# Optimization experiments

Hardware: AMD Instinct MI355X
Metric: run time of the kernel (lower is better)

Reference implementation:

```python
import jax, jax.numpy as jnp
import numpy as np

N = 50000   # nodes
E = 800000  # edges
B = 512     # graphs
EPS = 1e-5  # BatchNorm eps


def _p(k, shape, scale=0.05):
    return jax.random.normal(k, shape, dtype=jnp.float32) * scale


def setup_inputs() -> dict:
    key = jax.random.key(0)
    ks = jax.random.split(key, 24)
    inp = {
        "x": jax.random.normal(ks[0], (N, 4), dtype=jnp.float32),
        "edge_index": jax.random.randint(ks[1], (2, E), 0, N, dtype=jnp.int64),
        "edge_weight": jax.random.uniform(ks[2], (E,), dtype=jnp.float32),
        "batch": jnp.sort(jax.random.randint(ks[3], (N,), 0, B, dtype=jnp.int64)),
        # block1: GCNConv(4,64) + BN + shortcut Linear(4,64)
        "W1": _p(ks[4], (4, 64)), "b1": jnp.zeros((64,), jnp.float32),
        "g1": jnp.ones((64,), jnp.float32), "be1": jnp.zeros((64,), jnp.float32),
        "sW1": _p(ks[5], (4, 64)), "sb1": jnp.zeros((64,), jnp.float32),
        # block2: GCNConv(64,64) + BN, identity shortcut
        "W2": _p(ks[6], (64, 64)), "b2": jnp.zeros((64,), jnp.float32),
        "g2": jnp.ones((64,), jnp.float32), "be2": jnp.zeros((64,), jnp.float32),
        # block3: GCNConv(64,128) + BN + shortcut Linear(64,128)
        "W3": _p(ks[7], (64, 128)), "b3": jnp.zeros((128,), jnp.float32),
        "g3": jnp.ones((128,), jnp.float32), "be3": jnp.zeros((128,), jnp.float32),
        "sW3": _p(ks[8], (64, 128)), "sb3": jnp.zeros((128,), jnp.float32),
        # head: Linear(256,128) + BN + ReLU + Linear(128,1)
        "fW1": _p(ks[9], (256, 128)), "fb1": jnp.zeros((128,), jnp.float32),
        "fg": jnp.ones((128,), jnp.float32), "fbe": jnp.zeros((128,), jnp.float32),
        "fW2": _p(ks[10], (128, 1)), "fb2": jnp.zeros((1,), jnp.float32),
    }
    return inp


def _bn(x, g, b):
    # training-mode BatchNorm1d over node dim (biased variance)
    m = x.mean(0)
    v = x.var(0)
    return (x - m) * jax.lax.rsqrt(v + EPS) * g + b


def _gcn(x, W, b, src, dst, w, n):
    # PyG GCNConv: add self-loops (weight 1), symmetric normalization
    h = x @ W  # [n, out]
    loop = jnp.arange(n)
    s = jnp.concatenate([src, loop])
    d = jnp.concatenate([dst, loop])
    ww = jnp.concatenate([w, jnp.ones((n,), x.dtype)])
    deg = jax.ops.segment_sum(ww, d, num_segments=n)
    dis = jnp.where(deg > 0, jax.lax.rsqrt(jnp.maximum(deg, EPS)), 0.0)
    norm = dis[s] * ww * dis[d]  # [E+n]
    return jax.ops.segment_sum(h[s] * norm[:, None], d, num_segments=n) + b


def _block(x, W, b, g, be, sW, sb, src, dst, w, n):
    out = jax.nn.relu(_bn(_gcn(x, W, b, src, dst, w, n), g, be))
    sc = x if sW is None else x @ sW + sb
    return out + sc


def reference(x, edge_index, edge_weight, batch,
              W1, b1, g1, be1, sW1, sb1,
              W2, b2, g2, be2,
              W3, b3, g3, be3, sW3, sb3,
              fW1, fb1, fg, fbe, fW2, fb2):
    n = x.shape[0]
    src, dst = edge_index[0], edge_index[1]
    h = _block(x, W1, b1, g1, be1, sW1, sb1, src, dst, edge_weight, n)
    h = _block(h, W2, b2, g2, be2, None, None, src, dst, edge_weight, n)
    h = _block(h, W3, b3, g3, be3, sW3, sb3, src, dst, edge_weight, n)
    # global mean / max pooling per graph
    cnt = jax.ops.segment_sum(jnp.ones((n,), h.dtype), batch, num_segments=B)
    p1 = jax.ops.segment_sum(h, batch, num_segments=B) / jnp.maximum(cnt, 1.0)[:, None]
    p2 = jax.ops.segment_max(h, batch, num_segments=B)
    z = jnp.concatenate([p1, p2], axis=1)  # [B, 256]
    z = jax.nn.relu(_bn(z @ fW1 + fb1, fg, fbe))  # Dropout eval = identity
    return z @ fW2 + fb2  # [B, 1]
```

## Files before the change

### kernel.cpp

```cpp
#include <hip/hip_runtime.h>
#include <hip/hip_fp16.h>

#define BNEPS 1e-5f


__global__ void k_fill(float* p, int n, float v){
  int i = blockIdx.x*blockDim.x + threadIdx.x;
  if(i < n) p[i] = v;
}


__global__ void k_count(int* cnt, int* rank, const int* __restrict__ dst, int E){
  int e = blockIdx.x*blockDim.x + threadIdx.x;
  if(e < E) rank[e] = atomicAdd(&cnt[dst[e]], 1);
}

__global__ void k_scan1(const int* __restrict__ cnt, int* rowptr, int* bsum, int n){
  __shared__ int sh[256];
  int tid = threadIdx.x;
  int i = blockIdx.x*256 + tid;
  int v = (i < n) ? cnt[i] : 0;
  sh[tid] = v;
  __syncthreads();
  for(int o = 1; o < 256; o <<= 1){
    int t = (tid >= o) ? sh[tid-o] : 0;
    __syncthreads();
    sh[tid] += t;
    __syncthreads();
  }
  if(i < n) rowptr[i] = sh[tid] - v;
  if(tid == 255) bsum[blockIdx.x] = sh[255];
}

__global__ void k_scan2(int* bsum, int m){
  __shared__ int sh[256];
  int tid = threadIdx.x;
  int v = (tid < m) ? bsum[tid] : 0;
  sh[tid] = v;
  __syncthreads();
  for(int o = 1; o < 256; o <<= 1){
    int t = (tid >= o) ? sh[tid-o] : 0;
    __syncthreads();
    sh[tid] += t;
    __syncthreads();
  }
  if(tid < m) bsum[tid] = sh[tid] - v;
}

__global__ void k_scan3(int* rowptr, const int* bsum, int n, int E){
  int i = blockIdx.x*blockDim.x + threadIdx.x;
  if(i < n) rowptr[i] += bsum[i >> 8];
  if(i == 0) rowptr[n] = E;
}

__global__ void k_scatter2(const int* __restrict__ src, const int* __restrict__ dst,
                           const float* __restrict__ w, const int* __restrict__ rowptr,
                           const int* __restrict__ rank, int2* __restrict__ erec, int E){
  int e = blockIdx.x*blockDim.x + threadIdx.x;
  if(e >= E) return;
  int d = dst[e];
  erec[rowptr[d] + rank[e]] = make_int2(src[e], __float_as_int(w[e]));
}

__global__ void k_degdis(const int2* __restrict__ erec, const int* __restrict__ rowptr,
                         float* __restrict__ dis, int n){
  int i = blockIdx.x*blockDim.x + threadIdx.x;
  if(i >= n) return;
  float s = 1.0f;
  int e0 = rowptr[i], e1 = rowptr[i+1];
  for(int j = e0; j < e1; j++) s += __int_as_float(erec[j].y);
  dis[i] = rsqrtf(s);
}

__global__ void k_mknorm(int2* __restrict__ erec, const int* __restrict__ rowptr,
                         const float* __restrict__ dis, int n){
  int i = blockIdx.x*blockDim.x + threadIdx.x;
  if(i >= n) return;
  float di = dis[i];
  int e0 = rowptr[i], e1 = rowptr[i+1];
  for(int j = e0; j < e1; j++){
    int2 r = erec[j];
    erec[j].y = __float_as_int(dis[r.x] * __int_as_float(r.y) * di);
  }
}


__global__ __launch_bounds__(256)
void k_gcn1_fused(const float* __restrict__ X, const float* __restrict__ dis,
                  const int* __restrict__ rowptr, const int2* __restrict__ erec,
                  const float* __restrict__ W, const float* __restrict__ bias,
                  float* __restrict__ H, float* __restrict__ st1s, int n){
  const int tid = threadIdx.x;
  const int lane = tid & 63;
  const int wid = tid >> 6;
  const int eg = lane >> 2;
  const int ch = lane & 3;
  const float w0 = W[lane], w1 = W[64+lane], w2 = W[128+lane], w3 = W[192+lane];
  const float bc = bias[lane];
  float s = 0.f, s2 = 0.f;
  for(int i = blockIdx.x*4 + wid; i < n; i += gridDim.x*4){
    int e0 = rowptr[i], e1 = rowptr[i+1];
    float acc = 0.f;
    for(int j = e0 + eg; j < e1; j += 16){
      int2 r = erec[j];
      acc += X[(size_t)r.x*4 + ch] * __int_as_float(r.y);
    }
    if(eg == 0){
      float d = dis[i];
      acc += X[(size_t)i*4 + ch] * d * d;
    }
    acc += __shfl_xor(acc, 4);
    acc += __shfl_xor(acc, 8);
    acc += __shfl_xor(acc, 16);
    acc += __shfl_xor(acc, 32);
    float p0 = __shfl(acc, 0), p1 = __shfl(acc, 1);
    float p2 = __shfl(acc, 2), p3 = __shfl(acc, 3);
    float h = bc + p0*w0 + p1*w1 + p2*w2 + p3*w3;
    H[(size_t)i*64 + lane] = h;
    s += h; s2 += h*h;
  }
  __shared__ float rs[256], rs2[256];
  rs[tid] = s; rs2[tid] = s2;
  __syncthreads();
  if(tid < 64){
    float* stp = st1s + (blockIdx.x & 7)*128;
    atomicAdd(&stp[tid],    rs[tid]+rs[tid+64]+rs[tid+128]+rs[tid+192]);
    atomicAdd(&stp[64+tid], rs2[tid]+rs2[tid+64]+rs2[tid+128]+rs2[tid+192]);
  }
}


__global__ void k_gather64h(const __half* __restrict__ H, const float* __restrict__ dis,
                            const int* __restrict__ rowptr, const int2* __restrict__ erec,
                            float* __restrict__ P, int n){
  int i = blockIdx.x*4 + threadIdx.x / 64;
  int c = threadIdx.x & 63;
  if(i >= n) return;
  float di = dis[i];
  float acc = __half2float(H[(size_t)i*64 + c])*di*di;
  int e0 = rowptr[i], e1 = rowptr[i+1];
  int j = e0;
  for(; j + 8 <= e1; j += 8){
    int2 r0 = erec[j],   r1 = erec[j+1], r2 = erec[j+2], r3 = erec[j+3];
    int2 r4 = erec[j+4], r5 = erec[j+5], r6 = erec[j+6], r7 = erec[j+7];
    float h0 = __half2float(H[(size_t)r0.x*64 + c]);
    float h1 = __half2float(H[(size_t)r1.x*64 + c]);
    float h2 = __half2float(H[(size_t)r2.x*64 + c]);
    float h3 = __half2float(H[(size_t)r3.x*64 + c]);
    float h4 = __half2float(H[(size_t)r4.x*64 + c]);
    float h5 = __half2float(H[(size_t)r5.x*64 + c]);
    float h6 = __half2float(H[(size_t)r6.x*64 + c]);
    float h7 = __half2float(H[(size_t)r7.x*64 + c]);
    acc += h0*__int_as_float(r0.y) + h1*__int_as_float(r1.y)
         + h2*__int_as_float(r2.y) + h3*__int_as_float(r3.y)
         + h4*__int_as_float(r4.y) + h5*__int_as_float(r5.y)
         + h6*__int_as_float(r6.y) + h7*__int_as_float(r7.y);
  }
  for(; j < e1; j++){
    int2 r = erec[j];
    acc += __half2float(H[(size_t)r.x*64 + c]) * __int_as_float(r.y);
  }
  P[(size_t)i*64 + c] = acc;
}


template<int C>
__global__ __launch_bounds__(256)
void k_gemm_tile(const float* __restrict__ X, const float* __restrict__ W,
                 const float* __restrict__ bias, float* __restrict__ H,
                 float* __restrict__ stats, int n, int ntiles){
  const int RR = C/16;
  const int CG = C/4;
  __shared__ float Xs[64*65];
  __shared__ float Ws[64*C];
  __shared__ float sst[2*C];
  const int tid = threadIdx.x;
  const int cg = tid % CG, rg = tid / CG;
  const int c0 = cg*4;
  for(int t = tid; t < 16*C; t += 256)
    reinterpret_cast<float4*>(Ws)[t] = reinterpret_cast<const float4*>(W)[t];
  const float4 bc = *reinterpret_cast<const float4*>(bias + c0);
  float sacc[4] = {0,0,0,0}, qacc[4] = {0,0,0,0};
  const float4* X4 = reinterpret_cast<const float4*>(X);
  for(int tile = blockIdx.x; tile < ntiles; tile += gridDim.x){
    const int r0 = tile*64;
    __syncthreads();
    #pragma unroll
    for(int q = 0; q < 4; q++){
      int idx = tid + q*256;
      int row = idx >> 4, k4 = idx & 15;
      float4 v = (r0+row < n) ? X4[(size_t)(r0+row)*16 + k4] : make_float4(0.f,0.f,0.f,0.f);
      Xs[(4*k4+0)*65 + row] = v.x;
      Xs[(4*k4+1)*65 + row] = v.y;
      Xs[(4*k4+2)*65 + row] = v.z;
      Xs[(4*k4+3)*65 + row] = v.w;
    }
    __syncthreads();
    float acc[RR][4];
    #pragma unroll
    for(int r = 0; r < RR; r++){ acc[r][0]=bc.x; acc[r][1]=bc.y; acc[r][2]=bc.z; acc[r][3]=bc.w; }
    #pragma unroll 8
    for(int k = 0; k < 64; k++){
      float4 wv = reinterpret_cast<const float4*>(Ws)[k*CG + cg];
      #pragma unroll
      for(int r = 0; r < RR; r++){
        float xv = Xs[k*65 + rg*RR + r];
        acc[r][0] = fmaf(xv, wv.x, acc[r][0]);
        acc[r][1] = fmaf(xv, wv.y, acc[r][1]);
        acc[r][2] = fmaf(xv, wv.z, acc[r][2]);
        acc[r][3] = fmaf(xv, wv.w, acc[r][3]);
      }
    }
    #pragma unroll
    for(int r = 0; r < RR; r++){
      int row = r0 + rg*RR + r;
      if(row < n){
        *reinterpret_cast<float4*>(H + (size_t)row*C + c0) =
            make_float4(acc[r][0], acc[r][1], acc[r][2], acc[r][3]);
        #pragma unroll
        for(int j = 0; j < 4; j++){ sacc[j] += acc[r][j]; qacc[j] += acc[r][j]*acc[r][j]; }
      }
    }
  }
  for(int t = tid; t < 2*C; t += 256) sst[t] = 0.f;
  __syncthreads();
  #pragma unroll
  for(int j = 0; j < 4; j++){
    atomicAdd(&sst[c0+j], sacc[j]);
    atomicAdd(&sst[C+c0+j], qacc[j]);
  }
  __syncthreads();
  for(int t = tid; t < 2*C; t += 256) atomicAdd(&stats[t], sst[t]);
}

__global__ __launch_bounds__(256)
void k_gemm_bnsc_tile_h(const __half* __restrict__ Xh, const float* __restrict__ sW,
                        const float* __restrict__ sb,
                        const float* __restrict__ agg, const float* __restrict__ stats,
                        const float* __restrict__ g, const float* __restrict__ be,
                        float* __restrict__ out, int n, int ntiles){
  const int C = 128, RR = 8, CG = 32;
  __shared__ float Xs[64*65];
  __shared__ float Ws[64*C];
  const int tid = threadIdx.x;
  const int cg = tid % CG, rg = tid / CG;
  const int c0 = cg*4;
  for(int t = tid; t < 16*C; t += 256)
    reinterpret_cast<float4*>(Ws)[t] = reinterpret_cast<const float4*>(sW)[t];
  const float4 bc = *reinterpret_cast<const float4*>(sb + c0);
  float scal[4], shft[4];
  {
    float invn = 1.0f / n;
    #pragma unroll
    for(int j = 0; j < 4; j++){
      float m = stats[c0+j]*invn;
      float v = stats[C+c0+j]*invn - m*m;
      float rs = rsqrtf(v + BNEPS) * g[c0+j];
      scal[j] = rs;
      shft[j] = be[c0+j] - m*rs;
    }
  }
  for(int tile = blockIdx.x; tile < ntiles; tile += gridDim.x){
    const int r0 = tile*64;
    __syncthreads();
    #pragma unroll
    for(int q = 0; q < 2; q++){
      int t = tid + q*256;
      int row = t >> 3, h8 = t & 7;
      float4 raw = make_float4(0.f,0.f,0.f,0.f);
      if(r0+row < n) raw = *reinterpret_cast<const float4*>(Xh + (size_t)(r0+row)*64 + h8*8);
      const __half2* hp = reinterpret_cast<const __half2*>(&raw);
      #pragma unroll
      for(int p = 0; p < 4; p++){
        float2 f = __half22float2(hp[p]);
        Xs[(h8*8 + 2*p    )*65 + row] = f.x;
        Xs[(h8*8 + 2*p + 1)*65 + row] = f.y;
      }
    }
    __syncthreads();
    float acc[RR][4];
    #pragma unroll
    for(int r = 0; r < RR; r++){ acc[r][0]=bc.x; acc[r][1]=bc.y; acc[r][2]=bc.z; acc[r][3]=bc.w; }
    #pragma unroll 8
    for(int k = 0; k < 64; k++){
      float4 wv = reinterpret_cast<const float4*>(Ws)[k*CG + cg];
      #pragma unroll
      for(int r = 0; r < RR; r++){
        float xv = Xs[k*65 + rg*RR + r];
        acc[r][0] = fmaf(xv, wv.x, acc[r][0]);
        acc[r][1] = fmaf(xv, wv.y, acc[r][1]);
        acc[r][2] = fmaf(xv, wv.z, acc[r][2]);
        acc[r][3] = fmaf(xv, wv.w, acc[r][3]);
      }
    }
    #pragma unroll
    for(int r = 0; r < RR; r++){
      int row = r0 + rg*RR + r;
      if(row < n){
        float4 a = *reinterpret_cast<const float4*>(agg + (size_t)row*C + c0);
        float4 o;
        o.x = fmaxf(a.x*scal[0] + shft[0], 0.f) + acc[r][0];
        o.y = fmaxf(a.y*scal[1] + shft[1], 0.f) + acc[r][1];
        o.z = fmaxf(a.z*scal[2] + shft[2], 0.f) + acc[r][2];
        o.w = fmaxf(a.w*scal[3] + shft[3], 0.f) + acc[r][3];
        *reinterpret_cast<float4*>(out + (size_t)row*C + c0) = o;
      }
    }
  }
}


__global__ void k_bn_add4_h(const float* __restrict__ agg, const float* __restrict__ stats,
                            const float* __restrict__ g, const float* __restrict__ be,
                            __half* __restrict__ buf, int n){
  int idx = blockIdx.x*blockDim.x + threadIdx.x;
  if(idx >= n*16) return;
  int c = (idx & 15)*4;
  float invn = 1.0f / n;
  float4 sm = *reinterpret_cast<const float4*>(stats + c);
  float4 sq = *reinterpret_cast<const float4*>(stats + 64 + c);
  float4 g4 = *reinterpret_cast<const float4*>(g + c);
  float4 b4 = *reinterpret_cast<const float4*>(be + c);
  float4 a  = reinterpret_cast<const float4*>(agg)[idx];
  __half2* bp = reinterpret_cast<__half2*>(buf) + idx*2;
  float2 ad01 = __half22float2(bp[0]);
  float2 ad23 = __half22float2(bp[1]);
  float o0,o1,o2,o3;
  { float m=sm.x*invn, v=sq.x*invn-m*m; o0 = fmaxf((a.x-m)*rsqrtf(v+BNEPS)*g4.x+b4.x,0.f)+ad01.x; }
  { float m=sm.y*invn, v=sq.y*invn-m*m; o1 = fmaxf((a.y-m)*rsqrtf(v+BNEPS)*g4.y+b4.y,0.f)+ad01.y; }
  { float m=sm.z*invn, v=sq.z*invn-m*m; o2 = fmaxf((a.z-m)*rsqrtf(v+BNEPS)*g4.z+b4.z,0.f)+ad23.x; }
  { float m=sm.w*invn, v=sq.w*invn-m*m; o3 = fmaxf((a.w-m)*rsqrtf(v+BNEPS)*g4.w+b4.w,0.f)+ad23.y; }
  bp[0] = __floats2half2_rn(o0,o1);
  bp[1] = __floats2half2_rn(o2,o3);
}

__global__ void k_bn_sc4_h(const float* __restrict__ agg, const float* __restrict__ st1s,
                           const float* __restrict__ g, const float* __restrict__ be,
                           const float* __restrict__ X, const float* __restrict__ sW,
                           const float* __restrict__ sb, __half* __restrict__ out, int n){
  int idx = blockIdx.x*blockDim.x + threadIdx.x;
  if(idx >= n*16) return;
  int i = idx >> 4;
  int c = (idx & 15)*4;
  float invn = 1.0f / n;
  float4 xr = *reinterpret_cast<const float4*>(X + (size_t)i*4);
  float4 s0 = *reinterpret_cast<const float4*>(sW + c);
  float4 s1 = *reinterpret_cast<const float4*>(sW + 64 + c);
  float4 s2 = *reinterpret_cast<const float4*>(sW + 128 + c);
  float4 s3 = *reinterpret_cast<const float4*>(sW + 192 + c);
  float4 sb4 = *reinterpret_cast<const float4*>(sb + c);
  float4 sm = make_float4(0.f,0.f,0.f,0.f), sq = make_float4(0.f,0.f,0.f,0.f);
  #pragma unroll
  for(int sh = 0; sh < 8; sh++){
    float4 a4 = *reinterpret_cast<const float4*>(st1s + sh*128 + c);
    float4 b4 = *reinterpret_cast<const float4*>(st1s + sh*128 + 64 + c);
    sm.x += a4.x; sm.y += a4.y; sm.z += a4.z; sm.w += a4.w;
    sq.x += b4.x; sq.y += b4.y; sq.z += b4.z; sq.w += b4.w;
  }
  float4 g4 = *reinterpret_cast<const float4*>(g + c);
  float4 b4 = *reinterpret_cast<const float4*>(be + c);
  float4 a  = reinterpret_cast<const float4*>(agg)[idx];
  float o0,o1,o2,o3;
  #define BN1(X_, O_) { float sc = xr.x*s0.X_ + xr.y*s1.X_ + xr.z*s2.X_ + xr.w*s3.X_ + sb4.X_; \
    float m = sm.X_*invn; float v = sq.X_*invn - m*m; \
    O_ = fmaxf((a.X_-m)*rsqrtf(v+BNEPS)*g4.X_ + b4.X_, 0.f) + sc; }
  BN1(x,o0) BN1(y,o1) BN1(z,o2) BN1(w,o3)
  #undef BN1
  __half2* op = reinterpret_cast<__half2*>(out) + idx*2;
  op[0] = __floats2half2_rn(o0,o1);
  op[1] = __floats2half2_rn(o2,o3);
}


__global__ void k_pool(const float* __restrict__ H, const int* __restrict__ batch,
                       float* __restrict__ z, int n){
  int b = blockIdx.x, c = threadIdx.x;
  int lo = 0, hi = n;
  while(lo < hi){ int mid = (lo+hi)>>1; if(batch[mid] <  b) lo = mid+1; else hi = mid; }
  int start = lo;
  hi = n;
  while(lo < hi){ int mid = (lo+hi)>>1; if(batch[mid] <  b+1) lo = mid+1; else hi = mid; }
  int end = lo;
  float s = 0.f, mx = -INFINITY;
  for(int i = start; i < end; i++){
    float v = H[(size_t)i*128 + c];
    s += v; mx = fmaxf(mx, v);
  }
  int cnt = end - start;
  z[b*256 + c]       = s / fmaxf((float)cnt, 1.f);
  z[b*256 + 128 + c] = mx;
}

__global__ void k_head1(const float* __restrict__ z, const float* __restrict__ fW1,
                        const float* __restrict__ fb1, float* __restrict__ zr,
                        float* __restrict__ stats, int B){
  int idx = blockIdx.x*blockDim.x + threadIdx.x;
  int tid = threadIdx.x;
  float acc = 0.f;
  if(idx < B*128){
    int b = idx >> 7, c = idx & 127;
    acc = fb1[c];
    #pragma unroll 4
    for(int k = 0; k < 256; k++) acc = fmaf(z[b*256+k], fW1[k*128+c], acc);
    zr[idx] = acc;
  }
  __shared__ float rs[256], rs2[256];
  rs[tid] = acc; rs2[tid] = acc*acc;
  __syncthreads();
  if(tid < 128){
    atomicAdd(&stats[tid],     rs[tid]+rs[tid+128]);
    atomicAdd(&stats[128+tid], rs2[tid]+rs2[tid+128]);
  }
}

__global__ void k_final(const float* __restrict__ zr, const float* __restrict__ stats,
                        const float* __restrict__ fg, const float* __restrict__ fbe,
                        const float* __restrict__ fW2, const float* __restrict__ fb2,
                        float* __restrict__ out, int B){
  __shared__ float red[128];
  int b = blockIdx.x, c = threadIdx.x;
  float invn = 1.0f / B;
  float m  = stats[c]*invn;
  float v  = stats[128+c]*invn - m*m;
  float rs = rsqrtf(v + BNEPS);
  float val = fmaxf((zr[b*128+c]-m)*rs*fg[c] + fbe[c], 0.f) * fW2[c];
  red[c] = val;
  __syncthreads();
  for(int s = 64; s > 0; s >>= 1){
    if(c < s) red[c] += red[c+s];
    __syncthreads();
  }
  if(c == 0) out[b] = red[0] + fb2[0];
}


extern "C" void kernel_launch(void* const* d_in, const int* in_sizes, int n_in,
                              void* d_out, int out_size, void* d_ws, size_t ws_size,
                              hipStream_t stream){
  const float* x   = (const float*)d_in[0];
  const int*   ei  = (const int*)  d_in[1];
  const float* ew  = (const float*)d_in[2];
  const int*   bat = (const int*)  d_in[3];
  const float* W1  = (const float*)d_in[4];  const float* b1  = (const float*)d_in[5];
  const float* g1  = (const float*)d_in[6];  const float* be1 = (const float*)d_in[7];
  const float* sW1 = (const float*)d_in[8];  const float* sb1 = (const float*)d_in[9];
  const float* W2  = (const float*)d_in[10]; const float* b2  = (const float*)d_in[11];
  const float* g2  = (const float*)d_in[12]; const float* be2 = (const float*)d_in[13];
  const float* W3  = (const float*)d_in[14]; const float* b3  = (const float*)d_in[15];
  const float* g3  = (const float*)d_in[16]; const float* be3 = (const float*)d_in[17];
  const float* sW3 = (const float*)d_in[18]; const float* sb3 = (const float*)d_in[19];
  const float* fW1 = (const float*)d_in[20]; const float* fb1 = (const float*)d_in[21];
  const float* fg  = (const float*)d_in[22]; const float* fbe = (const float*)d_in[23];
  const float* fW2 = (const float*)d_in[24]; const float* fb2 = (const float*)d_in[25];
  float* out = (float*)d_out;

  const int n = in_sizes[0] / 4;
  const int E = in_sizes[2];
  const int B = out_size;
  const int* src = ei;
  const int* dst = ei + E;

  auto GB = [](long long t){ return (int)((t + 255) / 256); };
  const int nscanb = (n + 255) / 256;
  const int ntiles = (n + 63) / 64;

  float* ws = (float*)d_ws;
  size_t off = 0;
  auto alloc = [&](size_t cnt)->float*{ float* p = ws + off; off += (cnt + 63) & ~size_t(63); return p; };

  const size_t npad = ((size_t)n + 63) & ~size_t(63);
  __half* bufA = (__half*)alloc((size_t)n * 32);
  float* hbuf  = alloc((size_t)n * 128);
  float* agg   = alloc((size_t)n * 128);
  float* z     = alloc((size_t)B * 256);
  float* zr    = alloc((size_t)B * 128);
  float* zreg  = alloc(npad + 1024 + 768);
  int*   cnt   = (int*)zreg;
  float* st1s = zreg + npad;
  float* st2  = st1s + 1024;
  float* st3  = st2 + 256;
  float* stH  = st3 + 256;
  float* dis    = alloc(n);
  int*   rowptr = (int*)alloc(n + 1);
  int*   bsum   = (int*)alloc(256);
  int*   rank   = (int*)alloc(E);
  int2*  erec   = (int2*)alloc((size_t)E * 2);

  k_fill<<<GB(npad + 1024 + 768),256,0,stream>>>(zreg, (int)(npad + 1024 + 768), 0.f);
  k_count<<<GB(E),256,0,stream>>>(cnt, rank, dst, E);
  k_scan1<<<nscanb,256,0,stream>>>(cnt, rowptr, bsum, n);
  k_scan2<<<1,256,0,stream>>>(bsum, nscanb);
  k_scan3<<<GB(n),256,0,stream>>>(rowptr, bsum, n, E);
  k_scatter2<<<GB(E),256,0,stream>>>(src, dst, ew, rowptr, rank, erec, E);
  k_degdis<<<GB(n),256,0,stream>>>(erec, rowptr, dis, n);
  k_mknorm<<<GB(n),256,0,stream>>>(erec, rowptr, dis, n);

  float* P = hbuf;
  k_gcn1_fused<<<2048,256,0,stream>>>(x, dis, rowptr, erec, W1, b1, agg, st1s, n);
  k_bn_sc4_h<<<GB((long long)n*16),256,0,stream>>>(agg, st1s, g1, be1, x, sW1, sb1, bufA, n);

  k_gather64h<<<(n+3)/4,256,0,stream>>>(bufA, dis, rowptr, erec, P, n);
  k_gemm_tile<64><<<512,256,0,stream>>>(P, W2, b2, agg, st2, n, ntiles);
  k_bn_add4_h<<<GB((long long)n*16),256,0,stream>>>(agg, st2, g2, be2, bufA, n);

  k_gather64h<<<(n+3)/4,256,0,stream>>>(bufA, dis, rowptr, erec, P, n);
  k_gemm_tile<128><<<512,256,0,stream>>>(P, W3, b3, agg, st3, n, ntiles);
  k_gemm_bnsc_tile_h<<<512,256,0,stream>>>(bufA, sW3, sb3, agg, st3, g3, be3, hbuf, n, ntiles);

  k_pool<<<B,128,0,stream>>>(hbuf, bat, z, n);
  k_head1<<<GB((long long)B*128),256,0,stream>>>(z, fW1, fb1, zr, stH, B);
  k_final<<<B,128,0,stream>>>(zr, stH, fg, fbe, fW2, fb2, out, B);
}
```

Measured before the change: 429.7 us.

## Pack edge count and fixed-point degree into one 64-bit atomic, fold norm into scatter

```diff
diff --git a/kernel.cpp b/kernel.cpp
--- a/kernel.cpp
+++ b/kernel.cpp
@@ -2,6 +2,7 @@
 #include <hip/hip_fp16.h>
 
 #define BNEPS 1e-5f
+#define DEGFIX 16777216.0f
 
 
 __global__ void k_fill(float* p, int n, float v){
@@ -10,16 +11,27 @@
 }
 
 
-__global__ void k_count(int* cnt, int* rank, const int* __restrict__ dst, int E){
+__global__ void k_count64(unsigned long long* cnt64, int* rank,
+                          const int* __restrict__ dst, const float* __restrict__ w, int E){
   int e = blockIdx.x*blockDim.x + threadIdx.x;
-  if(e < E) rank[e] = atomicAdd(&cnt[dst[e]], 1);
-}
-
-__global__ void k_scan1(const int* __restrict__ cnt, int* rowptr, int* bsum, int n){
+  if(e >= E) return;
+  unsigned long long add = (1ull << 40) | (unsigned long long)(w[e] * DEGFIX);
+  unsigned long long old = atomicAdd(&cnt64[dst[e]], add);
+  rank[e] = (int)(old >> 40);
+}
+
+__global__ void k_scan1(const unsigned long long* __restrict__ cnt64, float* __restrict__ dis,
+                        int* rowptr, int* bsum, int n){
   __shared__ int sh[256];
   int tid = threadIdx.x;
   int i = blockIdx.x*256 + tid;
-  int v = (i < n) ? cnt[i] : 0;
+  int v = 0;
+  if(i < n){
+    unsigned long long val = cnt64[i];
+    v = (int)(val >> 40);
+    float deg = (float)(val & ((1ull<<40)-1)) * (1.0f/DEGFIX);
+    dis[i] = rsqrtf(1.0f + deg);
+  }
   sh[tid] = v;
   __syncthreads();
   for(int o = 1; o < 256; o <<= 1){
@@ -55,33 +67,14 @@
 
 __global__ void k_scatter2(const int* __restrict__ src, const int* __restrict__ dst,
                            const float* __restrict__ w, const int* __restrict__ rowptr,
-                           const int* __restrict__ rank, int2* __restrict__ erec, int E){
+                           const int* __restrict__ rank, const float* __restrict__ dis,
+                           int2* __restrict__ erec, int E){
   int e = blockIdx.x*blockDim.x + threadIdx.x;
   if(e >= E) return;
   int d = dst[e];
-  erec[rowptr[d] + rank[e]] = make_int2(src[e], __float_as_int(w[e]));
-}
-
-__global__ void k_degdis(const int2* __restrict__ erec, const int* __restrict__ rowptr,
-                         float* __restrict__ dis, int n){
-  int i = blockIdx.x*blockDim.x + threadIdx.x;
-  if(i >= n) return;
-  float s = 1.0f;
-  int e0 = rowptr[i], e1 = rowptr[i+1];
-  for(int j = e0; j < e1; j++) s += __int_as_float(erec[j].y);
-  dis[i] = rsqrtf(s);
-}
-
-__global__ void k_mknorm(int2* __restrict__ erec, const int* __restrict__ rowptr,
-                         const float* __restrict__ dis, int n){
-  int i = blockIdx.x*blockDim.x + threadIdx.x;
-  if(i >= n) return;
-  float di = dis[i];
-  int e0 = rowptr[i], e1 = rowptr[i+1];
-  for(int j = e0; j < e1; j++){
-    int2 r = erec[j];
-    erec[j].y = __float_as_int(dis[r.x] * __int_as_float(r.y) * di);
-  }
+  int s = src[e];
+  float nm = dis[s] * w[e] * dis[d];
+  erec[rowptr[d] + rank[e]] = make_int2(s, __float_as_int(nm));
 }
 
 
@@ -474,9 +467,9 @@
   float* agg   = alloc((size_t)n * 128);
   float* z     = alloc((size_t)B * 256);
   float* zr    = alloc((size_t)B * 128);
-  float* zreg  = alloc(npad + 1024 + 768);
-  int*   cnt   = (int*)zreg;
-  float* st1s = zreg + npad;
+  float* zreg  = alloc(2*npad + 1024 + 768);
+  unsigned long long* cnt64 = (unsigned long long*)zreg;
+  float* st1s = zreg + 2*npad;
   float* st2  = st1s + 1024;
   float* st3  = st2 + 256;
   float* stH  = st3 + 256;
@@ -486,14 +479,12 @@
   int*   rank   = (int*)alloc(E);
   int2*  erec   = (int2*)alloc((size_t)E * 2);
 
-  k_fill<<<GB(npad + 1024 + 768),256,0,stream>>>(zreg, (int)(npad + 1024 + 768), 0.f);
-  k_count<<<GB(E),256,0,stream>>>(cnt, rank, dst, E);
-  k_scan1<<<nscanb,256,0,stream>>>(cnt, rowptr, bsum, n);
+  k_fill<<<GB(2*npad + 1024 + 768),256,0,stream>>>(zreg, (int)(2*npad + 1024 + 768), 0.f);
+  k_count64<<<GB(E),256,0,stream>>>(cnt64, rank, dst, ew, E);
+  k_scan1<<<nscanb,256,0,stream>>>(cnt64, dis, rowptr, bsum, n);
   k_scan2<<<1,256,0,stream>>>(bsum, nscanb);
   k_scan3<<<GB(n),256,0,stream>>>(rowptr, bsum, n, E);
-  k_scatter2<<<GB(E),256,0,stream>>>(src, dst, ew, rowptr, rank, erec, E);
-  k_degdis<<<GB(n),256,0,stream>>>(erec, rowptr, dis, n);
-  k_mknorm<<<GB(n),256,0,stream>>>(erec, rowptr, dis, n);
+  k_scatter2<<<GB(E),256,0,stream>>>(src, dst, ew, rowptr, rank, dis, erec, E);
 
   float* P = hbuf;
   k_gcn1_fused<<<2048,256,0,stream>>>(x, dis, rowptr, erec, W1, b1, agg, st1s, n);
```

Result: faster. 419.1 us (-2.5%).
